# Kernel optimization log

Measured on AMD Instinct MI355X. Metric: run time of the kernel, lower is better.

Reference implementation:

```python
import jax, jax.numpy as jnp
import numpy as np

B, H, S, DK = 2, 16, 2048, 64


def setup_inputs() -> dict:
    key = jax.random.key(0)
    kq, kk, kv = jax.random.split(key, 3)
    query = jax.random.normal(kq, (B, H, S, DK), dtype=jnp.float32)
    k = jax.random.normal(kk, (B, H, S, DK), dtype=jnp.float32)
    value = jax.random.normal(kv, (B, H, S, DK), dtype=jnp.float32)
    # causal padding-style mask: 1 = keep, 0 = masked (set to -inf pre-softmax)
    mask = jnp.tril(jnp.ones((S, S), dtype=jnp.int32))[None, None, :, :]
    return {"query": query, "key": k, "value": value, "d_k": DK, "mask": mask}


def reference(query, key, value, d_k, mask):
    # scores: [B, H, Sq, Sk]
    scores = jnp.einsum("bhqd,bhkd->bhqk", query, key)
    scores = scores / jnp.sqrt(jnp.asarray(d_k, dtype=scores.dtype))
    scores = jnp.where(mask == 0, -jnp.inf, scores)
    att = jax.nn.softmax(scores, axis=-1)
    # dropout is identity in eval mode (deterministic reference)
    out = jnp.einsum("bhqk,bhkd->bhqd", att, value)
    return out
```

## Files before the change

### kernel.cpp

```cpp
#include <hip/hip_runtime.h>
#include <cstdint>

#define B_ 2
#define H_ 16
#define S_ 2048
#define DK_ 64
#define BH_ (B_*H_)
#define NQT 32

typedef __attribute__((ext_vector_type(8))) short short8;
typedef __attribute__((ext_vector_type(4))) short short4v;
typedef __attribute__((ext_vector_type(4))) float floatx4;

__device__ inline unsigned short f2bf(float f) {
  union { float f; unsigned u; } v; v.f = f;
  unsigned u = v.u;
  unsigned r = u + 0x7fffu + ((u >> 16) & 1u);
  return (unsigned short)(r >> 16);
}

__device__ inline floatx4 mfma16(short4v a, short4v b, floatx4 c) {
#if __has_builtin(__builtin_amdgcn_mfma_f32_16x16x16bf16_1k)
  return __builtin_amdgcn_mfma_f32_16x16x16bf16_1k(a, b, c, 0, 0, 0);
#else
  asm("v_mfma_f32_16x16x16_bf16 %0, %1, %2, %0" : "+v"(c) : "v"(a), "v"(b));
  return c;
#endif
}

__device__ inline short4v u2s4(unsigned a, unsigned b) {
  union { unsigned u[2]; short4v s; } v;
  v.u[0] = a; v.u[1] = b;
  return v.s;
}

__global__ __launch_bounds__(256) void conv_kv(const float* __restrict__ K,
                                               const float* __restrict__ V,
                                               unsigned short* __restrict__ Kb,
                                               unsigned short* __restrict__ Vb) {
  __shared__ __align__(16) unsigned short t[64 * 80];
  const int bh = blockIdx.y, s0 = blockIdx.x * 64;
  const int row = threadIdx.x >> 2, cp = threadIdx.x & 3;

  {
    const float* src = K + ((size_t)(bh * S_ + s0 + row)) * DK_ + cp * 16;
    unsigned short* dst = Kb + ((size_t)(bh * S_ + s0 + row)) * DK_ + cp * 16;
    #pragma unroll
    for (int h = 0; h < 2; ++h) {
      float4 a = *(const float4*)(src + h * 8);
      float4 b = *(const float4*)(src + h * 8 + 4);
      uint4 st;
      st.x = (unsigned)f2bf(a.x) | ((unsigned)f2bf(a.y) << 16);
      st.y = (unsigned)f2bf(a.z) | ((unsigned)f2bf(a.w) << 16);
      st.z = (unsigned)f2bf(b.x) | ((unsigned)f2bf(b.y) << 16);
      st.w = (unsigned)f2bf(b.z) | ((unsigned)f2bf(b.w) << 16);
      *(uint4*)(dst + h * 8) = st;
    }
  }
  {
    const float* src = V + ((size_t)(bh * S_ + s0 + row)) * DK_ + cp * 16;
    #pragma unroll
    for (int j4 = 0; j4 < 4; ++j4) {
      float4 a = *(const float4*)(src + j4 * 4);
      int c = cp * 16 + j4 * 4;
      t[(c + 0) * 80 + row] = f2bf(a.x);
      t[(c + 1) * 80 + row] = f2bf(a.y);
      t[(c + 2) * 80 + row] = f2bf(a.z);
      t[(c + 3) * 80 + row] = f2bf(a.w);
    }
    __syncthreads();
    const int base128 = s0 & ~127;
    const int t2 = 2 * ((s0 >> 6) & 1) + (cp >> 1);
    const int h  = cp & 1;
    unsigned short* dst = Vb + ((size_t)(bh * DK_ + row)) * S_ + base128 + t2 * 32 + h * 4;
    #pragma unroll
    for (int q = 0; q < 4; ++q)
      *(uint2*)(dst + q * 8) = *(const uint2*)&t[row * 80 + cp * 16 + q * 4];
  }
}

__global__ __launch_bounds__(256, 2)
void fa_kernel(const float* __restrict__ Q, const unsigned short* __restrict__ Kb,
               const unsigned short* __restrict__ Vb, float* __restrict__ Out) {
  __shared__ __align__(16) unsigned short Kt[2][8192];
  __shared__ __align__(16) unsigned short Vt[2][8192];

  const int tid  = threadIdx.x;
  const int wave = tid >> 6;
  const int lane = tid & 63;
  const int quad = lane >> 4;
  const int l16  = lane & 15;
  const int wq   = wave & 1;
  const int ws   = wave >> 1;

  const int id = blockIdx.x;
  const int bh = (id & 7) | (((id >> 3) & 3) << 3);
  const int qa = id >> 5;
  const int qb = NQT - 1 - qa;

  const float SCL = 0.125f * 1.44269504088896340736f;

  short8 qfB[4], qfA[4];
  auto loadQ = [&](int qt, short8* qf) {
    #pragma unroll
    for (int nq = 0; nq < 2; ++nq) {
      const float* p = Q + ((size_t)bh * S_ + qt * 64 + wq * 32 + nq * 16 + l16) * DK_ + quad * 8;
      #pragma unroll
      for (int ks = 0; ks < 2; ++ks) {
        float4 x = *(const float4*)(p + ks * 32);
        float4 y = *(const float4*)(p + ks * 32 + 4);
        short8 t;
        t[0]=(short)f2bf(x.x*SCL); t[1]=(short)f2bf(x.y*SCL); t[2]=(short)f2bf(x.z*SCL); t[3]=(short)f2bf(x.w*SCL);
        t[4]=(short)f2bf(y.x*SCL); t[5]=(short)f2bf(y.y*SCL); t[6]=(short)f2bf(y.z*SCL); t[7]=(short)f2bf(y.w*SCL);
        qf[nq * 2 + ks] = t;
      }
    }
  };
  loadQ(qb, qfB);
  loadQ(qa, qfA);

  floatx4 OtB[4][2], OtA[4][2];
  float lB_[2] = {0.f, 0.f}, lA_[2] = {0.f, 0.f};
  #pragma unroll
  for (int d = 0; d < 4; ++d)
    #pragma unroll
    for (int nq = 0; nq < 2; ++nq) { OtB[d][nq] = (floatx4){0,0,0,0}; OtA[d][nq] = (floatx4){0,0,0,0}; }

  auto stage = [&](int buf, int kv) {
    #pragma unroll
    for (int rd = 0; rd < 4; ++rd) {
      const int cid = rd * 256 + wave * 64 + lane;
      {
        int row = cid >> 3, p = cid & 7, c = p ^ (row & 7);
        const unsigned short* g = Kb + (((size_t)bh * S_ + kv * 128 + row) << 6) + (c << 3);
        __builtin_amdgcn_global_load_lds(
            (const __attribute__((address_space(1))) void*)g,
            (__attribute__((address_space(3))) void*)&Kt[buf][(rd * 4 + wave) * 512], 16, 0, 0);
      }
      {
        int row = cid >> 4, p = cid & 15, c = p ^ (row & 15);
        const unsigned short* g = Vb + (((size_t)bh * DK_ + row) << 11) + kv * 128 + (c << 3);
        __builtin_amdgcn_global_load_lds(
            (const __attribute__((address_space(1))) void*)g,
            (__attribute__((address_space(3))) void*)&Vt[buf][(rd * 4 + wave) * 512], 16, 0, 0);
      }
    }
  };

  auto computeT = [&](const short8* qf, floatx4 (*Ot)[2], float* ls,
                      int qt, int kv, int cur, bool domask) {
    unsigned pk[4][2][2];
    #pragma unroll
    for (int nt = 0; nt < 4; ++nt) {
      const int row = ws * 64 + nt * 16 + l16;
      floatx4 s0 = (floatx4){0,0,0,0}, s1 = (floatx4){0,0,0,0};
      #pragma unroll
      for (int ks = 0; ks < 2; ++ks) {
        const int p = (ks * 4 + quad) ^ (row & 7);
        const short8 ak = *(const short8*)&Kt[cur][row * 64 + p * 8];
        s0 = __builtin_amdgcn_mfma_f32_16x16x32_bf16(ak, qf[ks],     s0, 0, 0, 0);
        s1 = __builtin_amdgcn_mfma_f32_16x16x32_bf16(ak, qf[2 + ks], s1, 0, 0, 0);
      }
      if (domask) {
        const int sb  = kv * 128 + ws * 64 + nt * 16 + quad * 4;
        const int q0r = qt * 64 + wq * 32 + l16;
        #pragma unroll
        for (int r = 0; r < 4; ++r) {
          if (sb + r > q0r)      s0[r] = -INFINITY;
          if (sb + r > q0r + 16) s1[r] = -INFINITY;
        }
      }
      #pragma unroll
      for (int nq = 0; nq < 2; ++nq) {
        const floatx4 sv = nq ? s1 : s0;
        float e0 = __builtin_amdgcn_exp2f(sv[0]);
        float e1 = __builtin_amdgcn_exp2f(sv[1]);
        float e2 = __builtin_amdgcn_exp2f(sv[2]);
        float e3 = __builtin_amdgcn_exp2f(sv[3]);
        ls[nq] += (e0 + e1) + (e2 + e3);
        pk[nt][nq][0] = __builtin_amdgcn_perm(__float_as_uint(e1) + 0x8000u,
                                              __float_as_uint(e0) + 0x8000u, 0x07060302u);
        pk[nt][nq][1] = __builtin_amdgcn_perm(__float_as_uint(e3) + 0x8000u,
                                              __float_as_uint(e2) + 0x8000u, 0x07060302u);
      }
    }
    #pragma unroll
    for (int dblk = 0; dblk < 4; ++dblk) {
      const int row = dblk * 16 + l16;
      #pragma unroll
      for (int tt = 0; tt < 2; ++tt) {
        const int p = ((ws * 2 + tt) * 4 + quad) ^ l16;
        const short8 v8 = *(const short8*)&Vt[cur][row * 128 + p * 8];
        const short4v vlo = __builtin_shufflevector(v8, v8, 0, 1, 2, 3);
        const short4v vhi = __builtin_shufflevector(v8, v8, 4, 5, 6, 7);
        #pragma unroll
        for (int nq = 0; nq < 2; ++nq) {
          Ot[dblk][nq] = mfma16(vlo, u2s4(pk[2*tt  ][nq][0], pk[2*tt  ][nq][1]), Ot[dblk][nq]);
          Ot[dblk][nq] = mfma16(vhi, u2s4(pk[2*tt+1][nq][0], pk[2*tt+1][nq][1]), Ot[dblk][nq]);
        }
      }
    }
  };

  stage(0, 0);
  __syncthreads();
  const int nkvB = (qb + 2) >> 1;
  const int nkvA = (qa + 2) >> 1;
  for (int kv = 0; kv < nkvB; ++kv) {
    const int cur = kv & 1;
    if (kv + 1 < nkvB) stage(cur ^ 1, kv + 1);
    computeT(qfB, OtB, lB_, qb, kv, cur, kv == nkvB - 1);
    if (kv < nkvA) computeT(qfA, OtA, lA_, qa, kv, cur, kv == nkvA - 1);
    __syncthreads();
  }

  #pragma unroll
  for (int nq = 0; nq < 2; ++nq) {
    lB_[nq] += __shfl_xor(lB_[nq], 16); lB_[nq] += __shfl_xor(lB_[nq], 32);
    lA_[nq] += __shfl_xor(lA_[nq], 16); lA_[nq] += __shfl_xor(lA_[nq], 32);
  }
  float* OP = (float*)&Kt[0][0];
  float* LP = (float*)&Vt[0][0];
  if (ws == 1) {
    #pragma unroll
    for (int tile = 0; tile < 2; ++tile) {
      floatx4 (*Ot)[2] = tile ? OtA : OtB;
      const float* ls  = tile ? lA_ : lB_;
      #pragma unroll
      for (int nq = 0; nq < 2; ++nq) {
        const int rowi = ((wq * 2 + tile) * 2 + nq) * 16 + l16;
        #pragma unroll
        for (int dblk = 0; dblk < 4; ++dblk) {
          const int c2 = (dblk * 4 + quad) ^ (l16 & 12);
          *(floatx4*)&OP[rowi * 64 + c2 * 4] = Ot[dblk][nq];
        }
        if (quad == 0) LP[rowi] = ls[nq];
      }
    }
  }
  __syncthreads();
  if (ws == 0) {
    #pragma unroll
    for (int tile = 0; tile < 2; ++tile) {
      floatx4 (*Ot)[2] = tile ? OtA : OtB;
      const float* ls  = tile ? lA_ : lB_;
      const int qt     = tile ? qa : qb;
      #pragma unroll
      for (int nq = 0; nq < 2; ++nq) {
        const int rowi = ((wq * 2 + tile) * 2 + nq) * 16 + l16;
        const float inv = 1.0f / (ls[nq] + LP[rowi]);
        float* og = Out + ((size_t)bh * S_ + qt * 64 + wq * 32 + nq * 16 + l16) * DK_;
        #pragma unroll
        for (int dblk = 0; dblk < 4; ++dblk) {
          const int c2 = (dblk * 4 + quad) ^ (l16 & 12);
          floatx4 tot = Ot[dblk][nq] + *(const floatx4*)&OP[rowi * 64 + c2 * 4];
          tot *= inv;
          *(floatx4*)(og + dblk * 16 + quad * 4) = tot;
        }
      }
    }
  }
}

extern "C" void kernel_launch(void* const* d_in, const int* in_sizes, int n_in,
                              void* d_out, int out_size, void* d_ws, size_t ws_size,
                              hipStream_t stream) {
  const float* Q = (const float*)d_in[0];
  const float* K = (const float*)d_in[1];
  const float* V = (const float*)d_in[2];
  float* Out = (float*)d_out;
  unsigned short* Kb = (unsigned short*)d_ws;
  unsigned short* Vb = Kb + (size_t)BH_ * S_ * DK_;
  conv_kv<<<dim3(S_ / 64, BH_), 256, 0, stream>>>(K, V, Kb, Vb);
  fa_kernel<<<dim3(512), 256, 0, stream>>>(Q, Kb, Vb, Out);
}
```

Baseline: 140.0 us.

## Give each block one query tile with 64-wide KV tiles and skip masked subtiles

Replaces the paired-query-tile scheme, where each block took two q tiles and split each 128-wide KV tile across wave pairs before a shared-memory merge. Now each block owns one 64-row q tile, each wave owns 16 query rows, and KV is streamed in 64-wide tiles. This removes the cross-wave reduction and halves LDS use so occupancy can rise (launch bounds raised to 4 blocks per CU), and on the diagonal tile the fully masked subtiles are skipped. It also adds setprio around the PV MFMAs. The trade-offs are less K/V reuse per LDS load, since each wave now covers only 16 rows, and uneven per-block work that depends on scheduling to balance.

```diff
diff --git a/kernel.cpp b/kernel.cpp
--- a/kernel.cpp
+++ b/kernel.cpp
@@ -79,67 +79,59 @@
   }
 }
 
-__global__ __launch_bounds__(256, 2)
+__global__ __launch_bounds__(256, 4)
 void fa_kernel(const float* __restrict__ Q, const unsigned short* __restrict__ Kb,
                const unsigned short* __restrict__ Vb, float* __restrict__ Out) {
-  __shared__ __align__(16) unsigned short Kt[2][8192];
-  __shared__ __align__(16) unsigned short Vt[2][8192];
+  __shared__ __align__(16) unsigned short Kt[2][4096];
+  __shared__ __align__(16) unsigned short Vt[2][4096];
 
   const int tid  = threadIdx.x;
   const int wave = tid >> 6;
   const int lane = tid & 63;
   const int quad = lane >> 4;
   const int l16  = lane & 15;
-  const int wq   = wave & 1;
-  const int ws   = wave >> 1;
+  const int wq   = wave;
 
   const int id = blockIdx.x;
   const int bh = (id & 7) | (((id >> 3) & 3) << 3);
-  const int qa = id >> 5;
-  const int qb = NQT - 1 - qa;
+  const int qt = id >> 5;
+  const int nkv = qt + 1;
 
   const float SCL = 0.125f * 1.44269504088896340736f;
 
-  short8 qfB[4], qfA[4];
-  auto loadQ = [&](int qt, short8* qf) {
-    #pragma unroll
-    for (int nq = 0; nq < 2; ++nq) {
-      const float* p = Q + ((size_t)bh * S_ + qt * 64 + wq * 32 + nq * 16 + l16) * DK_ + quad * 8;
-      #pragma unroll
-      for (int ks = 0; ks < 2; ++ks) {
-        float4 x = *(const float4*)(p + ks * 32);
-        float4 y = *(const float4*)(p + ks * 32 + 4);
-        short8 t;
-        t[0]=(short)f2bf(x.x*SCL); t[1]=(short)f2bf(x.y*SCL); t[2]=(short)f2bf(x.z*SCL); t[3]=(short)f2bf(x.w*SCL);
-        t[4]=(short)f2bf(y.x*SCL); t[5]=(short)f2bf(y.y*SCL); t[6]=(short)f2bf(y.z*SCL); t[7]=(short)f2bf(y.w*SCL);
-        qf[nq * 2 + ks] = t;
-      }
-    }
-  };
-  loadQ(qb, qfB);
-  loadQ(qa, qfA);
-
-  floatx4 OtB[4][2], OtA[4][2];
-  float lB_[2] = {0.f, 0.f}, lA_[2] = {0.f, 0.f};
+  short8 qf[2];
+  {
+    const float* p = Q + ((size_t)bh * S_ + qt * 64 + wq * 16 + l16) * DK_ + quad * 8;
+    #pragma unroll
+    for (int ks = 0; ks < 2; ++ks) {
+      float4 x = *(const float4*)(p + ks * 32);
+      float4 y = *(const float4*)(p + ks * 32 + 4);
+      short8 t;
+      t[0]=(short)f2bf(x.x*SCL); t[1]=(short)f2bf(x.y*SCL); t[2]=(short)f2bf(x.z*SCL); t[3]=(short)f2bf(x.w*SCL);
+      t[4]=(short)f2bf(y.x*SCL); t[5]=(short)f2bf(y.y*SCL); t[6]=(short)f2bf(y.z*SCL); t[7]=(short)f2bf(y.w*SCL);
+      qf[ks] = t;
+    }
+  }
+
+  floatx4 Ot[4];
+  float ls = 0.f;
   #pragma unroll
-  for (int d = 0; d < 4; ++d)
-    #pragma unroll
-    for (int nq = 0; nq < 2; ++nq) { OtB[d][nq] = (floatx4){0,0,0,0}; OtA[d][nq] = (floatx4){0,0,0,0}; }
+  for (int d = 0; d < 4; ++d) Ot[d] = (floatx4){0,0,0,0};
 
   auto stage = [&](int buf, int kv) {
     #pragma unroll
-    for (int rd = 0; rd < 4; ++rd) {
+    for (int rd = 0; rd < 2; ++rd) {
       const int cid = rd * 256 + wave * 64 + lane;
+      const int row = cid >> 3;
+      const int c   = (cid & 7) ^ (row & 7);
       {
-        int row = cid >> 3, p = cid & 7, c = p ^ (row & 7);
-        const unsigned short* g = Kb + (((size_t)bh * S_ + kv * 128 + row) << 6) + (c << 3);
+        const unsigned short* g = Kb + (((size_t)bh * S_ + kv * 64 + row) << 6) + (c << 3);
         __builtin_amdgcn_global_load_lds(
             (const __attribute__((address_space(1))) void*)g,
             (__attribute__((address_space(3))) void*)&Kt[buf][(rd * 4 + wave) * 512], 16, 0, 0);
       }
       {
-        int row = cid >> 4, p = cid & 15, c = p ^ (row & 15);
-        const unsigned short* g = Vb + (((size_t)bh * DK_ + row) << 11) + kv * 128 + (c << 3);
+        const unsigned short* g = Vb + (((size_t)bh * DK_ + row) << 11) + kv * 64 + (c << 3);
         __builtin_amdgcn_global_load_lds(
             (const __attribute__((address_space(1))) void*)g,
             (__attribute__((address_space(3))) void*)&Vt[buf][(rd * 4 + wave) * 512], 16, 0, 0);
@@ -147,118 +139,72 @@
     }
   };
 
-  auto computeT = [&](const short8* qf, floatx4 (*Ot)[2], float* ls,
-                      int qt, int kv, int cur, bool domask) {
-    unsigned pk[4][2][2];
+  auto computeT = [&](int cur, bool domask) {
+    unsigned pk[4][2];
     #pragma unroll
     for (int nt = 0; nt < 4; ++nt) {
-      const int row = ws * 64 + nt * 16 + l16;
-      floatx4 s0 = (floatx4){0,0,0,0}, s1 = (floatx4){0,0,0,0};
+      if (domask && nt > wq) continue;
+      const int row = nt * 16 + l16;
+      floatx4 s0 = (floatx4){0,0,0,0};
       #pragma unroll
       for (int ks = 0; ks < 2; ++ks) {
-        const int p = (ks * 4 + quad) ^ (row & 7);
+        const int p = (ks * 4 + quad) ^ (l16 & 7);
         const short8 ak = *(const short8*)&Kt[cur][row * 64 + p * 8];
-        s0 = __builtin_amdgcn_mfma_f32_16x16x32_bf16(ak, qf[ks],     s0, 0, 0, 0);
-        s1 = __builtin_amdgcn_mfma_f32_16x16x32_bf16(ak, qf[2 + ks], s1, 0, 0, 0);
-      }
-      if (domask) {
-        const int sb  = kv * 128 + ws * 64 + nt * 16 + quad * 4;
-        const int q0r = qt * 64 + wq * 32 + l16;
+        s0 = __builtin_amdgcn_mfma_f32_16x16x32_bf16(ak, qf[ks], s0, 0, 0, 0);
+      }
+      if (domask && nt == wq) {
         #pragma unroll
-        for (int r = 0; r < 4; ++r) {
-          if (sb + r > q0r)      s0[r] = -INFINITY;
-          if (sb + r > q0r + 16) s1[r] = -INFINITY;
-        }
-      }
-      #pragma unroll
-      for (int nq = 0; nq < 2; ++nq) {
-        const floatx4 sv = nq ? s1 : s0;
-        float e0 = __builtin_amdgcn_exp2f(sv[0]);
-        float e1 = __builtin_amdgcn_exp2f(sv[1]);
-        float e2 = __builtin_amdgcn_exp2f(sv[2]);
-        float e3 = __builtin_amdgcn_exp2f(sv[3]);
-        ls[nq] += (e0 + e1) + (e2 + e3);
-        pk[nt][nq][0] = __builtin_amdgcn_perm(__float_as_uint(e1) + 0x8000u,
-                                              __float_as_uint(e0) + 0x8000u, 0x07060302u);
-        pk[nt][nq][1] = __builtin_amdgcn_perm(__float_as_uint(e3) + 0x8000u,
-                                              __float_as_uint(e2) + 0x8000u, 0x07060302u);
-      }
-    }
+        for (int r = 0; r < 4; ++r)
+          if (quad * 4 + r > l16) s0[r] = -INFINITY;
+      }
+      float e0 = __builtin_amdgcn_exp2f(s0[0]);
+      float e1 = __builtin_amdgcn_exp2f(s0[1]);
+      float e2 = __builtin_amdgcn_exp2f(s0[2]);
+      float e3 = __builtin_amdgcn_exp2f(s0[3]);
+      ls += (e0 + e1) + (e2 + e3);
+      pk[nt][0] = __builtin_amdgcn_perm(__float_as_uint(e1) + 0x8000u,
+                                        __float_as_uint(e0) + 0x8000u, 0x07060302u);
+      pk[nt][1] = __builtin_amdgcn_perm(__float_as_uint(e3) + 0x8000u,
+                                        __float_as_uint(e2) + 0x8000u, 0x07060302u);
+    }
+    __builtin_amdgcn_s_setprio(1);
     #pragma unroll
     for (int dblk = 0; dblk < 4; ++dblk) {
       const int row = dblk * 16 + l16;
       #pragma unroll
       for (int tt = 0; tt < 2; ++tt) {
-        const int p = ((ws * 2 + tt) * 4 + quad) ^ l16;
-        const short8 v8 = *(const short8*)&Vt[cur][row * 128 + p * 8];
+        if (domask && 2 * tt > wq) continue;
+        const int p = (tt * 4 + quad) ^ (l16 & 7);
+        const short8 v8 = *(const short8*)&Vt[cur][row * 64 + p * 8];
         const short4v vlo = __builtin_shufflevector(v8, v8, 0, 1, 2, 3);
         const short4v vhi = __builtin_shufflevector(v8, v8, 4, 5, 6, 7);
-        #pragma unroll
-        for (int nq = 0; nq < 2; ++nq) {
-          Ot[dblk][nq] = mfma16(vlo, u2s4(pk[2*tt  ][nq][0], pk[2*tt  ][nq][1]), Ot[dblk][nq]);
-          Ot[dblk][nq] = mfma16(vhi, u2s4(pk[2*tt+1][nq][0], pk[2*tt+1][nq][1]), Ot[dblk][nq]);
-        }
-      }
-    }
+        Ot[dblk] = mfma16(vlo, u2s4(pk[2*tt  ][0], pk[2*tt  ][1]), Ot[dblk]);
+        if (!(domask && 2 * tt + 1 > wq))
+          Ot[dblk] = mfma16(vhi, u2s4(pk[2*tt+1][0], pk[2*tt+1][1]), Ot[dblk]);
+      }
+    }
+    __builtin_amdgcn_s_setprio(0);
   };
 
   stage(0, 0);
   __syncthreads();
-  const int nkvB = (qb + 2) >> 1;
-  const int nkvA = (qa + 2) >> 1;
-  for (int kv = 0; kv < nkvB; ++kv) {
+  int kv = 0;
+  for (; kv < nkv - 1; ++kv) {
     const int cur = kv & 1;
-    if (kv + 1 < nkvB) stage(cur ^ 1, kv + 1);
-    computeT(qfB, OtB, lB_, qb, kv, cur, kv == nkvB - 1);
-    if (kv < nkvA) computeT(qfA, OtA, lA_, qa, kv, cur, kv == nkvA - 1);
+    stage(cur ^ 1, kv + 1);
+    computeT(cur, false);
     __syncthreads();
   }
-
+  computeT(kv & 1, true);
+
+  ls += __shfl_xor(ls, 16);
+  ls += __shfl_xor(ls, 32);
+  const float inv = 1.0f / ls;
+  float* og = Out + ((size_t)bh * S_ + qt * 64 + wq * 16 + l16) * DK_;
   #pragma unroll
-  for (int nq = 0; nq < 2; ++nq) {
-    lB_[nq] += __shfl_xor(lB_[nq], 16); lB_[nq] += __shfl_xor(lB_[nq], 32);
-    lA_[nq] += __shfl_xor(lA_[nq], 16); lA_[nq] += __shfl_xor(lA_[nq], 32);
-  }
-  float* OP = (float*)&Kt[0][0];
-  float* LP = (float*)&Vt[0][0];
-  if (ws == 1) {
-    #pragma unroll
-    for (int tile = 0; tile < 2; ++tile) {
-      floatx4 (*Ot)[2] = tile ? OtA : OtB;
-      const float* ls  = tile ? lA_ : lB_;
-      #pragma unroll
-      for (int nq = 0; nq < 2; ++nq) {
-        const int rowi = ((wq * 2 + tile) * 2 + nq) * 16 + l16;
-        #pragma unroll
-        for (int dblk = 0; dblk < 4; ++dblk) {
-          const int c2 = (dblk * 4 + quad) ^ (l16 & 12);
-          *(floatx4*)&OP[rowi * 64 + c2 * 4] = Ot[dblk][nq];
-        }
-        if (quad == 0) LP[rowi] = ls[nq];
-      }
-    }
-  }
-  __syncthreads();
-  if (ws == 0) {
-    #pragma unroll
-    for (int tile = 0; tile < 2; ++tile) {
-      floatx4 (*Ot)[2] = tile ? OtA : OtB;
-      const float* ls  = tile ? lA_ : lB_;
-      const int qt     = tile ? qa : qb;
-      #pragma unroll
-      for (int nq = 0; nq < 2; ++nq) {
-        const int rowi = ((wq * 2 + tile) * 2 + nq) * 16 + l16;
-        const float inv = 1.0f / (ls[nq] + LP[rowi]);
-        float* og = Out + ((size_t)bh * S_ + qt * 64 + wq * 32 + nq * 16 + l16) * DK_;
-        #pragma unroll
-        for (int dblk = 0; dblk < 4; ++dblk) {
-          const int c2 = (dblk * 4 + quad) ^ (l16 & 12);
-          floatx4 tot = Ot[dblk][nq] + *(const floatx4*)&OP[rowi * 64 + c2 * 4];
-          tot *= inv;
-          *(floatx4*)(og + dblk * 16 + quad * 4) = tot;
-        }
-      }
-    }
+  for (int dblk = 0; dblk < 4; ++dblk) {
+    floatx4 tot = Ot[dblk] * inv;
+    *(floatx4*)(og + dblk * 16 + quad * 4) = tot;
   }
 }
 
@@ -272,5 +218,5 @@
   unsigned short* Kb = (unsigned short*)d_ws;
   unsigned short* Vb = Kb + (size_t)BH_ * S_ * DK_;
   conv_kv<<<dim3(S_ / 64, BH_), 256, 0, stream>>>(K, V, Kb, Vb);
-  fa_kernel<<<dim3(512), 256, 0, stream>>>(Q, Kb, Vb, Out);
-}
+  fa_kernel<<<dim3(NQT * BH_), 256, 0, stream>>>(Q, Kb, Vb, Out);
+}
```

Result: slower. 145.8 us (+4.2%).
